# Optimization experiments

Measured on AMD Instinct MI355X. Metric: run time of the kernel, lower is better.

## Reference

```python
import jax, jax.numpy as jnp
import numpy as np

N = 102400      # total nodes across batch of graphs
E = 1638400     # edges (before self-loops)
G = 256         # number of graphs
F_IN = 64       # node_feat_dim
H = 4           # heads (conv1)
C = 32          # hidden per head
CLIN = 5
NEG_SLOPE = 0.2


def setup_inputs() -> dict:
    key = jax.random.key(0)
    ks = jax.random.split(key, 16)
    s = 0.1
    x = jax.random.normal(ks[0], (N, F_IN), jnp.float32)
    edge_index = jax.random.randint(ks[1], (2, E), 0, N, dtype=jnp.int32)
    batch = (jnp.arange(N, dtype=jnp.int32) * G) // N  # sorted graph ids, 400 nodes each
    clinical = jax.random.normal(ks[2], (G, CLIN), jnp.float32)
    W1 = jax.random.normal(ks[3], (F_IN, H * C), jnp.float32) * s
    a_src1 = jax.random.normal(ks[4], (H, C), jnp.float32) * s
    a_dst1 = jax.random.normal(ks[5], (H, C), jnp.float32) * s
    b1 = jnp.zeros((H * C,), jnp.float32)
    # GATConv 2: 128 -> 32, 1 head, no concat (mean over heads = identity for 1 head)
    W2 = jax.random.normal(ks[6], (H * C, C), jnp.float32) * s
    a_src2 = jax.random.normal(ks[7], (1, C), jnp.float32) * s
    a_dst2 = jax.random.normal(ks[8], (1, C), jnp.float32) * s
    b2 = jnp.zeros((C,), jnp.float32)
    # Classifier: Linear(37,16) -> ELU -> Linear(16,1)
    Wc1 = jax.random.normal(ks[9], (C + CLIN, 16), jnp.float32) * s
    bc1 = jnp.zeros((16,), jnp.float32)
    Wc2 = jax.random.normal(ks[10], (16, 1), jnp.float32) * s
    bc2 = jnp.zeros((1,), jnp.float32)
    return dict(x=x, edge_index=edge_index, batch=batch, clinical=clinical,
                W1=W1, a_src1=a_src1, a_dst1=a_dst1, b1=b1,
                W2=W2, a_src2=a_src2, a_dst2=a_dst2, b2=b2,
                Wc1=Wc1, bc1=bc1, Wc2=Wc2, bc2=bc2)


def _gat(x, W, a_src, a_dst, b, src, dst, heads, concat):
    n = x.shape[0]
    h = (x @ W).reshape(n, heads, -1)                 # [N, H, C]
    al_src = jnp.einsum('nhc,hc->nh', h, a_src)       # [N, H]
    al_dst = jnp.einsum('nhc,hc->nh', h, a_dst)
    e = jax.nn.leaky_relu(al_src[src] + al_dst[dst], NEG_SLOPE)  # [E, H]
    # segment softmax over incoming edges of each destination node
    m = jax.ops.segment_max(e, dst, num_segments=n)
    ex = jnp.exp(e - m[dst])
    den = jax.ops.segment_sum(ex, dst, num_segments=n)
    alpha = ex / den[dst]                             # [E, H]
    msg = h[src] * alpha[:, :, None]                  # [E, H, C]
    out = jax.ops.segment_sum(msg, dst, num_segments=n)
    out = out.reshape(n, -1) if concat else out.mean(axis=1)
    return out + b


def reference(x, edge_index, batch, clinical,
              W1, a_src1, a_dst1, b1, W2, a_src2, a_dst2, b2,
              Wc1, bc1, Wc2, bc2):
    n = x.shape[0]
    loop = jnp.arange(n, dtype=edge_index.dtype)
    src = jnp.concatenate([edge_index[0], loop])      # PyG add_self_loops=True
    dst = jnp.concatenate([edge_index[1], loop])
    h = _gat(x, W1, a_src1, a_dst1, b1, src, dst, H, True)   # [N, 128]
    h = jax.nn.elu(h)
    h = _gat(h, W2, a_src2, a_dst2, b2, src, dst, 1, False)  # [N, 32]
    h = jax.nn.elu(h)
    # global mean pool per graph
    sums = jax.ops.segment_sum(h, batch, num_segments=G)
    cnt = jax.ops.segment_sum(jnp.ones((n,), h.dtype), batch, num_segments=G)
    pooled = sums / cnt[:, None]                      # [G, 32]
    fused = jnp.concatenate([pooled, clinical.reshape(-1, CLIN)], axis=1)  # [G, 37]
    z = jax.nn.elu(fused @ Wc1 + bc1)
    return z @ Wc2 + bc2                              # [G, 1]
```

## Files before the change

### kernel.cpp

```cpp
#include <hip/hip_runtime.h>
#include <math.h>

#define N_NODES 102400
#define N_EDGES 1638400
#define G_GRAPHS 256
#define NODES_PER_G 400
#define CAPB 7168
#define F_IN  64
#define H1    4
#define C1    32
#define F_MID 128
#define C2    32
#define CLIN  5
#define NEG   0.2f

__device__ __forceinline__ float lrelu(float x) { return x > 0.f ? x : NEG * x; }
__device__ __forceinline__ float elu(float x)   { return x > 0.f ? x : expm1f(x); }

__device__ __forceinline__ unsigned short f2bf(float f) {
    unsigned u = __float_as_uint(f);
    u = (u + 0x7fffu + ((u >> 16) & 1u)) >> 16;
    return (unsigned short)u;
}
__device__ __forceinline__ float bfLO(unsigned p) { return __uint_as_float(p << 16); }
__device__ __forceinline__ float bfHI(unsigned p) { return __uint_as_float(p & 0xffff0000u); }
__device__ __forceinline__ float4 bf2f4(uint2 p) {
    return make_float4(__uint_as_float(p.x << 16), __uint_as_float(p.x & 0xffff0000u),
                       __uint_as_float(p.y << 16), __uint_as_float(p.y & 0xffff0000u));
}

__global__ __launch_bounds__(256) void bin_k(const int* __restrict__ ei,
                                             int* __restrict__ gcnt,
                                             unsigned* __restrict__ binned) {
    __shared__ int hist[256];
    __shared__ int off[256];
    int t = threadIdx.x;
    hist[t] = 0;
    __syncthreads();
    int i0 = blockIdx.x * 4096;
#pragma unroll
    for (int j = 0; j < 16; ++j) {
        int d = ei[N_EDGES + i0 + j * 256 + t];
        atomicAdd(&hist[d / NODES_PER_G], 1);
    }
    __syncthreads();
    off[t] = atomicAdd(&gcnt[t], hist[t]);
    hist[t] = 0;
    __syncthreads();
#pragma unroll
    for (int j = 0; j < 16; ++j) {
        int idx = i0 + j * 256 + t;
        int s = ei[idx];
        int d = ei[N_EDGES + idx];
        int g = d / NODES_PER_G;
        int dl = d - g * NODES_PER_G;
        int slot = atomicAdd(&hist[g], 1);
        binned[(size_t)g * CAPB + off[g] + slot] = (unsigned)s | ((unsigned)dl << 17);
    }
}

__global__ __launch_bounds__(512) void build_k(
    const int* __restrict__ gcnt, unsigned* __restrict__ binned,
    int* __restrict__ row_ptr, int* __restrict__ row_end)
{
    __shared__ unsigned edg[CAPB];
    __shared__ int coll[CAPB];
    __shared__ int hist[512];
    __shared__ int cur[NODES_PER_G];
    int g = blockIdx.x, t = threadIdx.x;
    int ne = gcnt[g];
    size_t base = (size_t)g * CAPB;
    for (int i = t; i < ne; i += 512) edg[i] = binned[base + i];
    hist[t] = 0;
    __syncthreads();
    for (int i = t; i < ne; i += 512) atomicAdd(&hist[edg[i] >> 17], 1);
    __syncthreads();
    int v = hist[t];
    for (int off = 1; off < 512; off <<= 1) {
        int tmp = (t >= off) ? hist[t - off] : 0;
        __syncthreads();
        hist[t] += tmp;
        __syncthreads();
    }
    int excl = hist[t] - v;
    if (t < NODES_PER_G) {
        cur[t] = excl;
        row_ptr[g * NODES_PER_G + t] = (int)base + excl;
    }
    __syncthreads();
    for (int i = t; i < ne; i += 512) {
        unsigned e = edg[i];
        int pos = atomicAdd(&cur[e >> 17], 1);
        coll[pos] = (int)(e & 0x1FFFFu);
    }
    __syncthreads();
    if (t < NODES_PER_G) row_end[g * NODES_PER_G + t] = (int)base + cur[t];
    for (int i = t; i < ne; i += 512) binned[base + i] = (unsigned)coll[i];
}

__global__ __launch_bounds__(256) void ht_k(
    const float* __restrict__ x, const float* __restrict__ W1,
    const float* __restrict__ a_src1, const float* __restrict__ a_dst1,
    unsigned short* __restrict__ hth, float* __restrict__ als1, float* __restrict__ ald1,
    float* __restrict__ pooled)
{
    __shared__ float xs[64 * 68];
    __shared__ float W1s[64 * 160];
    int t = threadIdx.x;
    int n0 = blockIdx.x * 64;
    if (blockIdx.x == 0) {
        for (int j = t; j < G_GRAPHS * C2; j += 256) pooled[j] = 0.f;
    }
#pragma unroll
    for (int j = 0; j < 4; ++j) {
        int q = t + 256 * j;
        int n = q >> 4, c0 = (q & 15) * 4;
        *(float4*)&xs[n * 68 + c0] = ((const float4*)x)[(size_t)n0 * 16 + q];
    }
#pragma unroll
    for (int j = 0; j < 8; ++j) {
        int q = t + 256 * j;
        int k = q >> 5, c0 = (q & 31) * 4;
        float4 v = ((const float4*)W1)[q];
        *(float4*)&W1s[k * 160 + (c0 >> 4) * 20 + (c0 & 15)] = v;
    }
    __syncthreads();
    int np = t >> 3;
    int nA = 2 * np, nB = nA + 1;
    int cg = t & 7;
    float accA[16], accB[16];
#pragma unroll
    for (int j = 0; j < 16; ++j) { accA[j] = 0.f; accB[j] = 0.f; }
    const float* wp = &W1s[cg * 20];
#pragma unroll 4
    for (int k = 0; k < F_IN; ++k) {
        float a = xs[nA * 68 + k];
        float b = xs[nB * 68 + k];
        const float* wr = wp + k * 160;
#pragma unroll
        for (int j = 0; j < 4; ++j) {
            float4 w = *(const float4*)(wr + 4 * j);
            accA[4 * j + 0] += a * w.x;
            accA[4 * j + 1] += a * w.y;
            accA[4 * j + 2] += a * w.z;
            accA[4 * j + 3] += a * w.w;
            accB[4 * j + 0] += b * w.x;
            accB[4 * j + 1] += b * w.y;
            accB[4 * j + 2] += b * w.z;
            accB[4 * j + 3] += b * w.w;
        }
    }
    int head = cg >> 1, hoff = (cg & 1) * 16;
    const float* asp = a_src1 + head * 32 + hoff;
    const float* adp = a_dst1 + head * 32 + hoff;
    float psA = 0.f, pdA = 0.f, psB = 0.f, pdB = 0.f;
#pragma unroll
    for (int j = 0; j < 16; ++j) {
        psA += accA[j] * asp[j]; pdA += accA[j] * adp[j];
        psB += accB[j] * asp[j]; pdB += accB[j] * adp[j];
    }
    psA += __shfl_xor(psA, 1);
    pdA += __shfl_xor(pdA, 1);
    psB += __shfl_xor(psB, 1);
    pdB += __shfl_xor(pdB, 1);
    if ((cg & 1) == 0) {
        als1[(size_t)(n0 + nA) * 4 + head] = psA;
        ald1[(size_t)(n0 + nA) * 4 + head] = pdA;
        als1[(size_t)(n0 + nB) * 4 + head] = psB;
        ald1[(size_t)(n0 + nB) * 4 + head] = pdB;
    }
    unsigned uA[8], uB[8];
#pragma unroll
    for (int j = 0; j < 8; ++j) {
        uA[j] = ((unsigned)f2bf(accA[2 * j + 1]) << 16) | (unsigned)f2bf(accA[2 * j]);
        uB[j] = ((unsigned)f2bf(accB[2 * j + 1]) << 16) | (unsigned)f2bf(accB[2 * j]);
    }
    uint4* hpA = (uint4*)(hth + ((size_t)(n0 + nA) * F_MID + cg * 16));
    hpA[0] = make_uint4(uA[0], uA[1], uA[2], uA[3]);
    hpA[1] = make_uint4(uA[4], uA[5], uA[6], uA[7]);
    uint4* hpB = (uint4*)(hth + ((size_t)(n0 + nB) * F_MID + cg * 16));
    hpB[0] = make_uint4(uB[0], uB[1], uB[2], uB[3]);
    hpB[1] = make_uint4(uB[4], uB[5], uB[6], uB[7]);
}

__global__ __launch_bounds__(256, 8) void agg1_k(
    const int* __restrict__ row_ptr, const int* __restrict__ row_end,
    const unsigned* __restrict__ col, const unsigned short* __restrict__ hth,
    const float* __restrict__ als1, const float* __restrict__ ald1,
    const float* __restrict__ b1, float* __restrict__ h1)
{
    int t = threadIdx.x;
    int wv = t >> 6, lane = t & 63, h = lane >> 4;
    int hw = (lane >> 3) & 3;
    int ew = lane & 7;
    int d = blockIdx.x * 4 + wv;
    const unsigned* hv = (const unsigned*)hth;

    float adv  = ald1[d * 4 + h];
    float advB = ald1[d * 4 + hw];
    float w = __expf(lrelu(als1[d * 4 + h] + adv));
    unsigned p = hv[(size_t)d * 64 + lane];
    float a0 = w * bfLO(p), a1 = w * bfHI(p);
    float den = w;

    int bidx = (h << 3);

    int e0 = __builtin_amdgcn_readfirstlane(row_ptr[d]);
    int e1 = __builtin_amdgcn_readfirstlane(row_end[d]);
    int e = e0;
    for (; e + 8 <= e1; e += 8) {
        unsigned sv = col[e + ew];
        int s0 = __builtin_amdgcn_readlane(sv, 0);
        int s1 = __builtin_amdgcn_readlane(sv, 1);
        int s2 = __builtin_amdgcn_readlane(sv, 2);
        int s3 = __builtin_amdgcn_readlane(sv, 3);
        int s4 = __builtin_amdgcn_readlane(sv, 4);
        int s5 = __builtin_amdgcn_readlane(sv, 5);
        int s6 = __builtin_amdgcn_readlane(sv, 6);
        int s7 = __builtin_amdgcn_readlane(sv, 7);
        unsigned p0 = hv[(size_t)s0 * 64 + lane];
        unsigned p1 = hv[(size_t)s1 * 64 + lane];
        unsigned p2 = hv[(size_t)s2 * 64 + lane];
        unsigned p3 = hv[(size_t)s3 * 64 + lane];
        unsigned p4 = hv[(size_t)s4 * 64 + lane];
        unsigned p5 = hv[(size_t)s5 * 64 + lane];
        unsigned p6 = hv[(size_t)s6 * 64 + lane];
        unsigned p7 = hv[(size_t)s7 * 64 + lane];
        float avv  = als1[(size_t)sv * 4 + hw];
        float wAll = __expf(lrelu(avv + advB));
        float w0 = __shfl(wAll, bidx + 0);
        float w1 = __shfl(wAll, bidx + 1);
        float w2 = __shfl(wAll, bidx + 2);
        float w3 = __shfl(wAll, bidx + 3);
        float w4 = __shfl(wAll, bidx + 4);
        float w5 = __shfl(wAll, bidx + 5);
        float w6 = __shfl(wAll, bidx + 6);
        float w7 = __shfl(wAll, bidx + 7);
        a0 += w0 * bfLO(p0) + w1 * bfLO(p1) + w2 * bfLO(p2) + w3 * bfLO(p3);
        a0 += w4 * bfLO(p4) + w5 * bfLO(p5) + w6 * bfLO(p6) + w7 * bfLO(p7);
        a1 += w0 * bfHI(p0) + w1 * bfHI(p1) + w2 * bfHI(p2) + w3 * bfHI(p3);
        a1 += w4 * bfHI(p4) + w5 * bfHI(p5) + w6 * bfHI(p6) + w7 * bfHI(p7);
        den += w0 + w1 + w2 + w3 + w4 + w5 + w6 + w7;
    }
    if (e < e1) {
        int iv = e + ew;
        bool inr = iv < e1;
        unsigned sv = col[inr ? iv : (e1 - 1)];
        int s0 = __builtin_amdgcn_readlane(sv, 0);
        int s1 = __builtin_amdgcn_readlane(sv, 1);
        int s2 = __builtin_amdgcn_readlane(sv, 2);
        int s3 = __builtin_amdgcn_readlane(sv, 3);
        int s4 = __builtin_amdgcn_readlane(sv, 4);
        int s5 = __builtin_amdgcn_readlane(sv, 5);
        int s6 = __builtin_amdgcn_readlane(sv, 6);
        int s7 = __builtin_amdgcn_readlane(sv, 7);
        unsigned p0 = hv[(size_t)s0 * 64 + lane];
        unsigned p1 = hv[(size_t)s1 * 64 + lane];
        unsigned p2 = hv[(size_t)s2 * 64 + lane];
        unsigned p3 = hv[(size_t)s3 * 64 + lane];
        unsigned p4 = hv[(size_t)s4 * 64 + lane];
        unsigned p5 = hv[(size_t)s5 * 64 + lane];
        unsigned p6 = hv[(size_t)s6 * 64 + lane];
        unsigned p7 = hv[(size_t)s7 * 64 + lane];
        float avv  = als1[(size_t)sv * 4 + hw];
        float wAll = inr ? __expf(lrelu(avv + advB)) : 0.f;
        float w0 = __shfl(wAll, bidx + 0);
        float w1 = __shfl(wAll, bidx + 1);
        float w2 = __shfl(wAll, bidx + 2);
        float w3 = __shfl(wAll, bidx + 3);
        float w4 = __shfl(wAll, bidx + 4);
        float w5 = __shfl(wAll, bidx + 5);
        float w6 = __shfl(wAll, bidx + 6);
        float w7 = __shfl(wAll, bidx + 7);
        a0 += w0 * bfLO(p0) + w1 * bfLO(p1) + w2 * bfLO(p2) + w3 * bfLO(p3);
        a0 += w4 * bfLO(p4) + w5 * bfLO(p5) + w6 * bfLO(p6) + w7 * bfLO(p7);
        a1 += w0 * bfHI(p0) + w1 * bfHI(p1) + w2 * bfHI(p2) + w3 * bfHI(p3);
        a1 += w4 * bfHI(p4) + w5 * bfHI(p5) + w6 * bfHI(p6) + w7 * bfHI(p7);
        den += w0 + w1 + w2 + w3 + w4 + w5 + w6 + w7;
    }
    float inv = 1.f / den;
    float2 bb = ((const float2*)b1)[lane];
    float2 o;
    o.x = elu(a0 * inv + bb.x);
    o.y = elu(a1 * inv + bb.y);
    ((float2*)h1)[(size_t)d * 64 + lane] = o;
}

__global__ __launch_bounds__(256) void dense2_k(
    const float* __restrict__ h1, const float* __restrict__ W2,
    const float* __restrict__ a_src2, const float* __restrict__ a_dst2,
    unsigned short* __restrict__ h2h, float* __restrict__ al_s2, float* __restrict__ al_d2)
{
    __shared__ float hs[64 * 132];
    __shared__ float W2s[128 * 32];
    __shared__ float h2s[64 * 36];
    int t = threadIdx.x;
    int n0 = blockIdx.x * 64;
#pragma unroll
    for (int j = 0; j < 8; ++j) {
        int q = t + 256 * j;
        int n = q >> 5, c0 = (q & 31) * 4;
        *(float4*)&hs[n * 132 + c0] = ((const float4*)h1)[(size_t)n0 * 32 + q];
    }
#pragma unroll
    for (int j = 0; j < 4; ++j) {
        int q = t + 256 * j;
        ((float4*)W2s)[q] = ((const float4*)W2)[q];
    }
    __syncthreads();
    int ng = t >> 3, og = t & 7;
    int nA = 2 * ng, nB = nA + 1;
    int o4 = og * 4;
    float4 aA = make_float4(0.f, 0.f, 0.f, 0.f);
    float4 aB = aA;
#pragma unroll 8
    for (int k = 0; k < F_MID; k += 4) {
        float4 hA = *(const float4*)&hs[nA * 132 + k];
        float4 hB = *(const float4*)&hs[nB * 132 + k];
        float4 w0 = *(const float4*)&W2s[(k + 0) * 32 + o4];
        float4 w1 = *(const float4*)&W2s[(k + 1) * 32 + o4];
        float4 w2 = *(const float4*)&W2s[(k + 2) * 32 + o4];
        float4 w3 = *(const float4*)&W2s[(k + 3) * 32 + o4];
        aA.x += hA.x * w0.x; aA.y += hA.x * w0.y; aA.z += hA.x * w0.z; aA.w += hA.x * w0.w;
        aA.x += hA.y * w1.x; aA.y += hA.y * w1.y; aA.z += hA.y * w1.z; aA.w += hA.y * w1.w;
        aA.x += hA.z * w2.x; aA.y += hA.z * w2.y; aA.z += hA.z * w2.z; aA.w += hA.z * w2.w;
        aA.x += hA.w * w3.x; aA.y += hA.w * w3.y; aA.z += hA.w * w3.z; aA.w += hA.w * w3.w;
        aB.x += hB.x * w0.x; aB.y += hB.x * w0.y; aB.z += hB.x * w0.z; aB.w += hB.x * w0.w;
        aB.x += hB.y * w1.x; aB.y += hB.y * w1.y; aB.z += hB.y * w1.z; aB.w += hB.y * w1.w;
        aB.x += hB.z * w2.x; aB.y += hB.z * w2.y; aB.z += hB.z * w2.z; aB.w += hB.z * w2.w;
        aB.x += hB.w * w3.x; aB.y += hB.w * w3.y; aB.z += hB.w * w3.z; aB.w += hB.w * w3.w;
    }
    unsigned loA = ((unsigned)f2bf(aA.y) << 16) | (unsigned)f2bf(aA.x);
    unsigned hiA = ((unsigned)f2bf(aA.w) << 16) | (unsigned)f2bf(aA.z);
    ((uint2*)h2h)[(((size_t)(n0 + nA)) * C2 + o4) >> 2] = make_uint2(loA, hiA);
    unsigned loB = ((unsigned)f2bf(aB.y) << 16) | (unsigned)f2bf(aB.x);
    unsigned hiB = ((unsigned)f2bf(aB.w) << 16) | (unsigned)f2bf(aB.z);
    ((uint2*)h2h)[(((size_t)(n0 + nB)) * C2 + o4) >> 2] = make_uint2(loB, hiB);
    *(float4*)&h2s[nA * 36 + o4] = aA;
    *(float4*)&h2s[nB * 36 + o4] = aB;
    __syncthreads();
    if (t < 128) {
        int which = t >> 6, nn = t & 63;
        const float* a = which ? a_dst2 : a_src2;
        float s = 0.f;
#pragma unroll
        for (int k = 0; k < C2; ++k) s += h2s[nn * 36 + k] * a[k];
        if (which) al_d2[n0 + nn] = s;
        else       al_s2[n0 + nn] = s;
    }
}

__global__ __launch_bounds__(256, 8) void gather2(
    const int* __restrict__ row_ptr, const int* __restrict__ row_end,
    const unsigned* __restrict__ col, const float* __restrict__ al_src,
    const float* __restrict__ al_dst, const unsigned short* __restrict__ h2h,
    const float* __restrict__ b2, const int* __restrict__ batch,
    float* __restrict__ pooled)
{
    __shared__ float sv[32][C2];
    int t = threadIdx.x;
    int r = t >> 3;
    int sub = t & 7;
    int lane = t & 63;
    int base = lane & 56;
    int d = blockIdx.x * 32 + r;
    const uint2* h2v = (const uint2*)h2h;

    float ad = al_dst[d];
    float wself = __expf(lrelu(al_src[d] + ad));
    float4 v = bf2f4(h2v[(size_t)d * 8 + sub]);
    float ax = wself * v.x, ay = wself * v.y, az = wself * v.z, aw = wself * v.w;
    float wsum = 0.f;
    int e0 = row_ptr[d], e1 = row_end[d];

    for (int e = e0; __any(e < e1); e += 8) {
        int ei = e + sub;
        bool valid = ei < e1;
        unsigned svv = col[valid ? ei : 0];
        float av = al_src[(int)svv];
        float w = valid ? __expf(lrelu(av + ad)) : 0.f;
        wsum += w;
#pragma unroll
        for (int i = 0; i < 8; ++i) {
            int   si = __shfl((int)svv, base + i);
            float wi = __shfl(w, base + i);
            float4 xi = bf2f4(h2v[(size_t)si * 8 + sub]);
            ax += wi * xi.x; ay += wi * xi.y; az += wi * xi.z; aw += wi * xi.w;
        }
    }
    wsum += __shfl_xor(wsum, 1);
    wsum += __shfl_xor(wsum, 2);
    wsum += __shfl_xor(wsum, 4);
    float den = wsum + wself;

    float inv = 1.f / den;
    const float4 bv = ((const float4*)b2)[sub];
    sv[r][4 * sub + 0] = elu(ax * inv + bv.x);
    sv[r][4 * sub + 1] = elu(ay * inv + bv.y);
    sv[r][4 * sub + 2] = elu(az * inv + bv.z);
    sv[r][4 * sub + 3] = elu(aw * inv + bv.w);
    __syncthreads();
    int d0 = blockIdx.x * 32;
    int g0 = batch[d0], g1 = batch[d0 + 31];
    if (t < 64) {
        int which = t >> 5, ch = t & 31;
        int g = which ? g1 : g0;
        if (which == 0 || g1 != g0) {
            float s = 0.f;
            for (int rr = 0; rr < 32; ++rr)
                if (batch[d0 + rr] == g) s += sv[rr][ch];
            atomicAdd(&pooled[g * C2 + ch], s);
        }
    }
}

__global__ __launch_bounds__(256) void head_k(
    const float* __restrict__ pooled, const float* __restrict__ clinical,
    const float* __restrict__ Wc1, const float* __restrict__ bc1,
    const float* __restrict__ Wc2, const float* __restrict__ bc2,
    float* __restrict__ out)
{
    int g = threadIdx.x;
    float fused[C2 + CLIN];
    const float inv = 1.f / 400.f;
#pragma unroll
    for (int c = 0; c < C2; ++c) fused[c] = pooled[g * C2 + c] * inv;
#pragma unroll
    for (int c = 0; c < CLIN; ++c) fused[C2 + c] = clinical[g * CLIN + c];
    float o = bc2[0];
#pragma unroll
    for (int j = 0; j < 16; ++j) {
        float acc = bc1[j];
#pragma unroll
        for (int k = 0; k < C2 + CLIN; ++k) acc += fused[k] * Wc1[k * 16 + j];
        o += (acc > 0.f ? acc : expm1f(acc)) * Wc2[j];
    }
    out[g] = o;
}

extern "C" void kernel_launch(void* const* d_in, const int* in_sizes, int n_in,
                              void* d_out, int out_size, void* d_ws, size_t ws_size,
                              hipStream_t stream) {
    const float* x        = (const float*)d_in[0];
    const int*   ei       = (const int*)  d_in[1];
    const int*   batch    = (const int*)  d_in[2];
    const float* clinical = (const float*)d_in[3];
    const float* W1       = (const float*)d_in[4];
    const float* a_src1   = (const float*)d_in[5];
    const float* a_dst1   = (const float*)d_in[6];
    const float* b1       = (const float*)d_in[7];
    const float* W2       = (const float*)d_in[8];
    const float* a_src2   = (const float*)d_in[9];
    const float* a_dst2   = (const float*)d_in[10];
    const float* b2       = (const float*)d_in[11];
    const float* Wc1      = (const float*)d_in[12];
    const float* bc1      = (const float*)d_in[13];
    const float* Wc2      = (const float*)d_in[14];
    const float* bc2      = (const float*)d_in[15];
    float* out = (float*)d_out;

    const size_t N = N_NODES;
    float* ws = (float*)d_ws;
    size_t off = 0;
    float* als1   = ws + off; off += N * 4;
    float* ald1   = ws + off; off += N * 4;
    float* al_s2  = ws + off; off += N;
    float* al_d2  = ws + off; off += N;
    float* pooled = ws + off; off += (size_t)G_GRAPHS * C2;
    unsigned short* hth = (unsigned short*)(ws + off); off += N * F_MID / 2;
    float* h1     = ws + off; off += N * F_MID;
    unsigned short* h2h = (unsigned short*)(ws + off); off += N * C2 / 2;
    int* row_ptr = (int*)(ws + off); off += N;
    int* row_end = (int*)(ws + off); off += N;
    int* gcnt    = (int*)(ws + off); off += 256;
    unsigned* binned = (unsigned*)(ws + off); off += (size_t)G_GRAPHS * CAPB;

    hipMemsetAsync(gcnt, 0, 256 * sizeof(int), stream);

    bin_k  <<<N_EDGES / 4096, 256, 0, stream>>>(ei, gcnt, binned);
    build_k<<<G_GRAPHS, 512, 0, stream>>>(gcnt, binned, row_ptr, row_end);

    ht_k<<<N_NODES / 64, 256, 0, stream>>>(x, W1, a_src1, a_dst1, hth, als1, ald1, pooled);

    agg1_k<<<N_NODES / 4, 256, 0, stream>>>(row_ptr, row_end, binned, hth, als1, ald1,
                                            b1, h1);

    dense2_k<<<N_NODES / 64, 256, 0, stream>>>(h1, W2, a_src2, a_dst2, h2h, al_s2, al_d2);

    gather2<<<N_NODES / 32, 256, 0, stream>>>(row_ptr, row_end, binned, al_s2, al_d2, h2h,
                                              b2, batch, pooled);

    head_k<<<1, G_GRAPHS, 0, stream>>>(pooled, clinical, Wc1, bc1, Wc2, bc2, out);
}
```

Before: 303.4 us.

## Store layer-1 features head-major and aggregate per head; fuse classifier head into gather2

Layer-1 bf16 features are now stored head-major, so each head's 32 channels for a node form a contiguous 64-byte row. The aggregation kernel runs one grid slice per head, with 16 lanes per destination node. Each lane loads one source index and weight, and these are broadcast by shuffles across 16 edges per iteration. The aim is to shrink per-edge gather size and make better use of cache locality within each head plane. Separately, the classifier head_k launch is removed and replaced by a last-block ticket in gather2, saving one kernel launch at the cost of an atomic and fences.

```diff
diff --git a/kernel.cpp b/kernel.cpp
--- a/kernel.cpp
+++ b/kernel.cpp
@@ -175,115 +175,66 @@
         uA[j] = ((unsigned)f2bf(accA[2 * j + 1]) << 16) | (unsigned)f2bf(accA[2 * j]);
         uB[j] = ((unsigned)f2bf(accB[2 * j + 1]) << 16) | (unsigned)f2bf(accB[2 * j]);
     }
-    uint4* hpA = (uint4*)(hth + ((size_t)(n0 + nA) * F_MID + cg * 16));
-    hpA[0] = make_uint4(uA[0], uA[1], uA[2], uA[3]);
-    hpA[1] = make_uint4(uA[4], uA[5], uA[6], uA[7]);
-    uint4* hpB = (uint4*)(hth + ((size_t)(n0 + nB) * F_MID + cg * 16));
-    hpB[0] = make_uint4(uB[0], uB[1], uB[2], uB[3]);
-    hpB[1] = make_uint4(uB[4], uB[5], uB[6], uB[7]);
+    unsigned* hu = (unsigned*)hth;
+    size_t bA = (size_t)head * (N_NODES * 16) + (size_t)(n0 + nA) * 16 + (cg & 1) * 8;
+    size_t bB = (size_t)head * (N_NODES * 16) + (size_t)(n0 + nB) * 16 + (cg & 1) * 8;
+    ((uint4*)(hu + bA))[0] = make_uint4(uA[0], uA[1], uA[2], uA[3]);
+    ((uint4*)(hu + bA))[1] = make_uint4(uA[4], uA[5], uA[6], uA[7]);
+    ((uint4*)(hu + bB))[0] = make_uint4(uB[0], uB[1], uB[2], uB[3]);
+    ((uint4*)(hu + bB))[1] = make_uint4(uB[4], uB[5], uB[6], uB[7]);
 }
 
 __global__ __launch_bounds__(256, 8) void agg1_k(
     const int* __restrict__ row_ptr, const int* __restrict__ row_end,
-    const unsigned* __restrict__ col, const unsigned short* __restrict__ hth,
+    const unsigned* __restrict__ col, const unsigned* __restrict__ hthu,
     const float* __restrict__ als1, const float* __restrict__ ald1,
     const float* __restrict__ b1, float* __restrict__ h1)
 {
+    const int BLKS_PER_H = N_NODES / 16;
+    int h  = blockIdx.x / BLKS_PER_H;
+    int db = blockIdx.x - h * BLKS_PER_H;
     int t = threadIdx.x;
-    int wv = t >> 6, lane = t & 63, h = lane >> 4;
-    int hw = (lane >> 3) & 3;
-    int ew = lane & 7;
-    int d = blockIdx.x * 4 + wv;
-    const unsigned* hv = (const unsigned*)hth;
-
-    float adv  = ald1[d * 4 + h];
-    float advB = ald1[d * 4 + hw];
-    float w = __expf(lrelu(als1[d * 4 + h] + adv));
-    unsigned p = hv[(size_t)d * 64 + lane];
-    float a0 = w * bfLO(p), a1 = w * bfHI(p);
-    float den = w;
-
-    int bidx = (h << 3);
-
-    int e0 = __builtin_amdgcn_readfirstlane(row_ptr[d]);
-    int e1 = __builtin_amdgcn_readfirstlane(row_end[d]);
-    int e = e0;
-    for (; e + 8 <= e1; e += 8) {
-        unsigned sv = col[e + ew];
-        int s0 = __builtin_amdgcn_readlane(sv, 0);
-        int s1 = __builtin_amdgcn_readlane(sv, 1);
-        int s2 = __builtin_amdgcn_readlane(sv, 2);
-        int s3 = __builtin_amdgcn_readlane(sv, 3);
-        int s4 = __builtin_amdgcn_readlane(sv, 4);
-        int s5 = __builtin_amdgcn_readlane(sv, 5);
-        int s6 = __builtin_amdgcn_readlane(sv, 6);
-        int s7 = __builtin_amdgcn_readlane(sv, 7);
-        unsigned p0 = hv[(size_t)s0 * 64 + lane];
-        unsigned p1 = hv[(size_t)s1 * 64 + lane];
-        unsigned p2 = hv[(size_t)s2 * 64 + lane];
-        unsigned p3 = hv[(size_t)s3 * 64 + lane];
-        unsigned p4 = hv[(size_t)s4 * 64 + lane];
-        unsigned p5 = hv[(size_t)s5 * 64 + lane];
-        unsigned p6 = hv[(size_t)s6 * 64 + lane];
-        unsigned p7 = hv[(size_t)s7 * 64 + lane];
-        float avv  = als1[(size_t)sv * 4 + hw];
-        float wAll = __expf(lrelu(avv + advB));
-        float w0 = __shfl(wAll, bidx + 0);
-        float w1 = __shfl(wAll, bidx + 1);
-        float w2 = __shfl(wAll, bidx + 2);
-        float w3 = __shfl(wAll, bidx + 3);
-        float w4 = __shfl(wAll, bidx + 4);
-        float w5 = __shfl(wAll, bidx + 5);
-        float w6 = __shfl(wAll, bidx + 6);
-        float w7 = __shfl(wAll, bidx + 7);
-        a0 += w0 * bfLO(p0) + w1 * bfLO(p1) + w2 * bfLO(p2) + w3 * bfLO(p3);
-        a0 += w4 * bfLO(p4) + w5 * bfLO(p5) + w6 * bfLO(p6) + w7 * bfLO(p7);
-        a1 += w0 * bfHI(p0) + w1 * bfHI(p1) + w2 * bfHI(p2) + w3 * bfHI(p3);
-        a1 += w4 * bfHI(p4) + w5 * bfHI(p5) + w6 * bfHI(p6) + w7 * bfHI(p7);
-        den += w0 + w1 + w2 + w3 + w4 + w5 + w6 + w7;
-    }
-    if (e < e1) {
-        int iv = e + ew;
-        bool inr = iv < e1;
-        unsigned sv = col[inr ? iv : (e1 - 1)];
-        int s0 = __builtin_amdgcn_readlane(sv, 0);
-        int s1 = __builtin_amdgcn_readlane(sv, 1);
-        int s2 = __builtin_amdgcn_readlane(sv, 2);
-        int s3 = __builtin_amdgcn_readlane(sv, 3);
-        int s4 = __builtin_amdgcn_readlane(sv, 4);
-        int s5 = __builtin_amdgcn_readlane(sv, 5);
-        int s6 = __builtin_amdgcn_readlane(sv, 6);
-        int s7 = __builtin_amdgcn_readlane(sv, 7);
-        unsigned p0 = hv[(size_t)s0 * 64 + lane];
-        unsigned p1 = hv[(size_t)s1 * 64 + lane];
-        unsigned p2 = hv[(size_t)s2 * 64 + lane];
-        unsigned p3 = hv[(size_t)s3 * 64 + lane];
-        unsigned p4 = hv[(size_t)s4 * 64 + lane];
-        unsigned p5 = hv[(size_t)s5 * 64 + lane];
-        unsigned p6 = hv[(size_t)s6 * 64 + lane];
-        unsigned p7 = hv[(size_t)s7 * 64 + lane];
-        float avv  = als1[(size_t)sv * 4 + hw];
-        float wAll = inr ? __expf(lrelu(avv + advB)) : 0.f;
-        float w0 = __shfl(wAll, bidx + 0);
-        float w1 = __shfl(wAll, bidx + 1);
-        float w2 = __shfl(wAll, bidx + 2);
-        float w3 = __shfl(wAll, bidx + 3);
-        float w4 = __shfl(wAll, bidx + 4);
-        float w5 = __shfl(wAll, bidx + 5);
-        float w6 = __shfl(wAll, bidx + 6);
-        float w7 = __shfl(wAll, bidx + 7);
-        a0 += w0 * bfLO(p0) + w1 * bfLO(p1) + w2 * bfLO(p2) + w3 * bfLO(p3);
-        a0 += w4 * bfLO(p4) + w5 * bfLO(p5) + w6 * bfLO(p6) + w7 * bfLO(p7);
-        a1 += w0 * bfHI(p0) + w1 * bfHI(p1) + w2 * bfHI(p2) + w3 * bfHI(p3);
-        a1 += w4 * bfHI(p4) + w5 * bfHI(p5) + w6 * bfHI(p6) + w7 * bfHI(p7);
-        den += w0 + w1 + w2 + w3 + w4 + w5 + w6 + w7;
-    }
-    float inv = 1.f / den;
-    float2 bb = ((const float2*)b1)[lane];
+    int grp = t >> 4;
+    int sub = t & 15;
+    int lane = t & 63;
+    int base = lane & 48;
+    int d = db * 16 + grp;
+    const unsigned* th = hthu + (size_t)h * (N_NODES * 16);
+
+    float adv = ald1[d * 4 + h];
+    float wself = __expf(lrelu(als1[d * 4 + h] + adv));
+    unsigned pself = th[(size_t)d * 16 + sub];
+    float a0 = wself * bfLO(pself);
+    float a1 = wself * bfHI(pself);
+    float wsum = 0.f;
+
+    int e0 = row_ptr[d], e1 = row_end[d];
+    for (int e = e0; __any(e < e1); e += 16) {
+        int ei = e + sub;
+        bool valid = ei < e1;
+        unsigned svv = col[valid ? ei : e0];
+        float av = als1[(size_t)svv * 4 + h];
+        float w = valid ? __expf(lrelu(av + adv)) : 0.f;
+        wsum += w;
+#pragma unroll
+        for (int i = 0; i < 16; ++i) {
+            int   si = __shfl((int)svv, base + i);
+            float wi = __shfl(w, base + i);
+            unsigned pi = th[(size_t)si * 16 + sub];
+            a0 += wi * bfLO(pi);
+            a1 += wi * bfHI(pi);
+        }
+    }
+    wsum += __shfl_xor(wsum, 1);
+    wsum += __shfl_xor(wsum, 2);
+    wsum += __shfl_xor(wsum, 4);
+    wsum += __shfl_xor(wsum, 8);
+    float inv = 1.f / (wsum + wself);
+    float2 bb = ((const float2*)b1)[h * 16 + sub];
     float2 o;
     o.x = elu(a0 * inv + bb.x);
     o.y = elu(a1 * inv + bb.y);
-    ((float2*)h1)[(size_t)d * 64 + lane] = o;
+    ((float2*)h1)[(size_t)d * 64 + h * 16 + sub] = o;
 }
 
 __global__ __launch_bounds__(256) void dense2_k(
@@ -355,9 +306,14 @@
     const unsigned* __restrict__ col, const float* __restrict__ al_src,
     const float* __restrict__ al_dst, const unsigned short* __restrict__ h2h,
     const float* __restrict__ b2, const int* __restrict__ batch,
-    float* __restrict__ pooled)
+    float* __restrict__ pooled, int* __restrict__ ticket,
+    const float* __restrict__ clinical,
+    const float* __restrict__ Wc1, const float* __restrict__ bc1,
+    const float* __restrict__ Wc2, const float* __restrict__ bc2,
+    float* __restrict__ out)
 {
     __shared__ float sv[32][C2];
+    __shared__ int lastFlag;
     int t = threadIdx.x;
     int r = t >> 3;
     int sub = t & 7;
@@ -412,30 +368,29 @@
             atomicAdd(&pooled[g * C2 + ch], s);
         }
     }
-}
-
-__global__ __launch_bounds__(256) void head_k(
-    const float* __restrict__ pooled, const float* __restrict__ clinical,
-    const float* __restrict__ Wc1, const float* __restrict__ bc1,
-    const float* __restrict__ Wc2, const float* __restrict__ bc2,
-    float* __restrict__ out)
-{
-    int g = threadIdx.x;
-    float fused[C2 + CLIN];
-    const float inv = 1.f / 400.f;
-#pragma unroll
-    for (int c = 0; c < C2; ++c) fused[c] = pooled[g * C2 + c] * inv;
-#pragma unroll
-    for (int c = 0; c < CLIN; ++c) fused[C2 + c] = clinical[g * CLIN + c];
-    float o = bc2[0];
-#pragma unroll
-    for (int j = 0; j < 16; ++j) {
-        float acc = bc1[j];
-#pragma unroll
-        for (int k = 0; k < C2 + CLIN; ++k) acc += fused[k] * Wc1[k * 16 + j];
-        o += (acc > 0.f ? acc : expm1f(acc)) * Wc2[j];
-    }
-    out[g] = o;
+    __threadfence();
+    __syncthreads();
+    if (t == 0) lastFlag = (atomicAdd(ticket, 1) == (int)gridDim.x - 1);
+    __syncthreads();
+    if (lastFlag) {
+        __threadfence();
+        int g = t;
+        float fused[C2 + CLIN];
+        const float invn = 1.f / 400.f;
+#pragma unroll
+        for (int c = 0; c < C2; ++c) fused[c] = pooled[g * C2 + c] * invn;
+#pragma unroll
+        for (int c = 0; c < CLIN; ++c) fused[C2 + c] = clinical[g * CLIN + c];
+        float o = bc2[0];
+#pragma unroll
+        for (int j = 0; j < 16; ++j) {
+            float acc = bc1[j];
+#pragma unroll
+            for (int k = 0; k < C2 + CLIN; ++k) acc += fused[k] * Wc1[k * 16 + j];
+            o += (acc > 0.f ? acc : expm1f(acc)) * Wc2[j];
+        }
+        out[g] = o;
+    }
 }
 
 extern "C" void kernel_launch(void* const* d_in, const int* in_sizes, int n_in,
@@ -472,23 +427,24 @@
     unsigned short* h2h = (unsigned short*)(ws + off); off += N * C2 / 2;
     int* row_ptr = (int*)(ws + off); off += N;
     int* row_end = (int*)(ws + off); off += N;
-    int* gcnt    = (int*)(ws + off); off += 256;
+    int* gcnt    = (int*)(ws + off); off += 512;
     unsigned* binned = (unsigned*)(ws + off); off += (size_t)G_GRAPHS * CAPB;
-
-    hipMemsetAsync(gcnt, 0, 256 * sizeof(int), stream);
+    int* ticket = gcnt + 256;
+
+    hipMemsetAsync(gcnt, 0, 512 * sizeof(int), stream);
 
     bin_k  <<<N_EDGES / 4096, 256, 0, stream>>>(ei, gcnt, binned);
     build_k<<<G_GRAPHS, 512, 0, stream>>>(gcnt, binned, row_ptr, row_end);
 
     ht_k<<<N_NODES / 64, 256, 0, stream>>>(x, W1, a_src1, a_dst1, hth, als1, ald1, pooled);
 
-    agg1_k<<<N_NODES / 4, 256, 0, stream>>>(row_ptr, row_end, binned, hth, als1, ald1,
-                                            b1, h1);
+    agg1_k<<<4 * (N_NODES / 16), 256, 0, stream>>>(row_ptr, row_end, binned,
+                                                   (const unsigned*)hth, als1, ald1,
+                                                   b1, h1);
 
     dense2_k<<<N_NODES / 64, 256, 0, stream>>>(h1, W2, a_src2, a_dst2, h2h, al_s2, al_d2);
 
     gather2<<<N_NODES / 32, 256, 0, stream>>>(row_ptr, row_end, binned, al_s2, al_d2, h2h,
-                                              b2, batch, pooled);
-
-    head_k<<<1, G_GRAPHS, 0, stream>>>(pooled, clinical, Wc1, bc1, Wc2, bc2, out);
-}
+                                              b2, batch, pooled, ticket,
+                                              clinical, Wc1, bc1, Wc2, bc2, out);
+}
```

Result: slower. 656.9 us (+116.5%).
